# Performance work log

Hardware: AMD Instinct MI355X
Metric: run time of the kernel (lower is better)

The kernel has to match this reference:

```python
import jax, jax.numpy as jnp
import numpy as np
from math import factorial, sqrt

# ---- configuration (matches init_kwargs) ----
MUL = 64
N = 32768
IRREPS1 = [(MUL, l) for l in range(3)]   # 64x0e + 64x1o + 64x2e
IRREPS2 = [(1, l) for l in range(3)]     # 1x0e + 1x1o + 1x2e (spherical harmonics)
IRREPS_OUT = [(MUL, l) for l in range(3)]
# (i_in1, i_in2, i_out) -- all parity/triangle-allowed uvw paths with l<=2
PATHS = [(0,0,0),(0,1,1),(0,2,2),(1,0,1),(1,1,0),(1,1,2),(1,2,1),(2,0,2),(2,1,1),(2,2,0),(2,2,2)]

# ---- real Clebsch-Gordan (e3nn convention: real basis, unit Frobenius norm) ----
def _su2_cg(j1, m1, j2, m2, j3, m3):
    if m3 != m1 + m2:
        return 0.0
    f = factorial
    vmin = max(-j1 + j2 + m3, -j1 + m1, 0)
    vmax = min(j2 + j3 + m1, j3 - j1 + j2, j3 + m3)
    C = sqrt((2*j3+1) * f(j3+j1-j2) * f(j3-j1+j2) * f(j1+j2-j3) * f(j3+m3) * f(j3-m3)
             / (f(j1+j2+j3+1) * f(j1-m1) * f(j1+m1) * f(j2-m2) * f(j2+m2)))
    S = 0.0
    for v in range(vmin, vmax + 1):
        S += (-1.0)**(v + j2 + m2) * f(j2+j3+m1-v) * f(j1-m1+v) / (f(v) * f(j3-j1+j2-v) * f(j3+m3-v) * f(v+j1-j2-m3))
    return C * S

def _su2_clebsch_gordan(j1, j2, j3):
    mat = np.zeros((2*j1+1, 2*j2+1, 2*j3+1))
    for m1 in range(-j1, j1+1):
        for m2 in range(-j2, j2+1):
            if abs(m1 + m2) <= j3:
                mat[j1+m1, j2+m2, j3+m1+m2] = _su2_cg(j1, m1, j2, m2, j3, m1+m2)
    return mat

def _change_basis_real_to_complex(l):
    q = np.zeros((2*l+1, 2*l+1), dtype=np.complex128)
    for m in range(-l, 0):
        q[l+m, l+abs(m)] = 1/sqrt(2)
        q[l+m, l-abs(m)] = -1j/sqrt(2)
    q[l, l] = 1
    for m in range(1, l+1):
        q[l+m, l+abs(m)] = (-1)**m / sqrt(2)
        q[l+m, l-abs(m)] = 1j * (-1)**m / sqrt(2)
    return (-1j)**l * q

def clebsch_gordan(l1, l2, l3):
    Q1 = _change_basis_real_to_complex(l1)
    Q2 = _change_basis_real_to_complex(l2)
    Q3 = _change_basis_real_to_complex(l3)
    C = _su2_clebsch_gordan(l1, l2, l3)
    C = np.einsum('ij,kl,mn,ikn->jlm', Q1, Q2, np.conj(Q3.T), C)
    C = np.real(C)
    return C / np.linalg.norm(C)  # unit Frobenius norm (e3nn convention)

# ---- static layout / path weights ----
def _offsets(irreps):
    offs, s = [], 0
    for mul, l in irreps:
        offs.append(s)
        s += mul * (2*l + 1)
    return offs

OFF1, OFF2, OFFO = _offsets(IRREPS1), _offsets(IRREPS2), _offsets(IRREPS_OUT)
# path_normalization='element', irrep_normalization='component'
_norm = {}
for (i1, i2, io) in PATHS:
    _norm[io] = _norm.get(io, 0) + IRREPS1[i1][0] * IRREPS2[i2][0]
PW = [sqrt((2*IRREPS_OUT[io][1] + 1) / _norm[io]) for (_, _, io) in PATHS]


def setup_inputs() -> dict:
    key = jax.random.key(0)
    k1, k2, k3 = jax.random.split(key, 3)
    dim1 = sum(m * (2*l+1) for m, l in IRREPS1)  # 576
    dim2 = sum(m * (2*l+1) for m, l in IRREPS2)  # 9
    nw = sum(IRREPS1[i1][0] * IRREPS2[i2][0] * IRREPS_OUT[io][0] for (i1, i2, io) in PATHS)
    x1 = jax.random.normal(k1, (N, dim1), dtype=jnp.float32)
    x2 = jax.random.normal(k2, (N, dim2), dtype=jnp.float32)
    weights = jax.random.normal(k3, (nw,), dtype=jnp.float32)
    return {"x1": x1, "x2": x2, "weights": weights}


def reference(x1, x2, weights):
    out_acc = [None] * len(IRREPS_OUT)
    wi = 0
    for (i1, i2, io), pw in zip(PATHS, PW):
        m1, l1 = IRREPS1[i1]
        m2, l2 = IRREPS2[i2]
        mo, lo = IRREPS_OUT[io]
        npar = m1 * m2 * mo
        w = weights[wi:wi + npar].reshape(m1, m2, mo)
        wi += npar
        # per-irrep chunks: [N, mul, 2l+1]
        x1c = x1[:, OFF1[i1]:OFF1[i1] + m1 * (2*l1+1)].reshape(-1, m1, 2*l1+1)
        x2c = x2[:, OFF2[i2]:OFF2[i2] + m2 * (2*l2+1)].reshape(-1, m2, 2*l2+1)
        cg = jnp.asarray(pw * clebsch_gordan(l1, l2, lo), dtype=x1.dtype)
        out = jnp.einsum('uvw,ijk,nui,nvj->nwk', w, cg, x1c, x2c)
        out_acc[io] = out if out_acc[io] is None else out_acc[io] + out
    return jnp.concatenate([o.reshape(o.shape[0], -1) for o in out_acc], axis=1)
```

## Files before the change

kernel.cpp:

```cpp
#include <hip/hip_runtime.h>
#include <hip/hip_bf16.h>

#define NDIM1 576
#define NDIM2 9
#define NDIMO 576

typedef __attribute__((ext_vector_type(8))) short short8;
typedef __attribute__((ext_vector_type(4))) float f32x4;

union U8 { unsigned short s[8]; short8 v; };

__device__ inline unsigned short f2bf(float x) {
  return __builtin_bit_cast(unsigned short, __float2bfloat16(x));
}

constexpr bool cg_nonzero(int m1, int m2, int m3) {
  int a1 = m1 < 0 ? -m1 : m1, a2 = m2 < 0 ? -m2 : m2, a3 = m3 < 0 ? -m3 : m3;
  int d = a1 > a2 ? a1 - a2 : a2 - a1;
  bool mag = (a3 == a1 + a2) || (a3 == d);
  int neg = (m1 < 0) + (m2 < 0) + (m3 < 0);
  return mag && ((neg & 1) == 0);
}

constexpr double cfact(int n) { double r = 1.0; for (int i = 2; i <= n; i++) r *= (double)i; return r; }
constexpr double csqrt_(double x) {
  if (x <= 0.0) return 0.0;
  double g = x < 1.0 ? 1.0 : x;
  for (int i = 0; i < 60; i++) g = 0.5 * (g + x / g);
  return g;
}
constexpr int cmax3(int a, int b, int c) { int m = a > b ? a : b; return m > c ? m : c; }
constexpr int cmin3(int a, int b, int c) { int m = a < b ? a : b; return m < c ? m : c; }

struct cpx { double re; double im; };
constexpr cpx operator*(cpx a, cpx b) { return {a.re * b.re - a.im * b.im, a.re * b.im + a.im * b.re}; }
constexpr cpx operator+(cpx a, cpx b) { return {a.re + b.re, a.im + b.im}; }
constexpr cpx cconj(cpx a) { return {a.re, -a.im}; }
constexpr cpx cscale(cpx a, double s) { return {a.re * s, a.im * s}; }

constexpr double su2_cg_c(int j1, int m1, int j2, int m2, int j3, int m3) {
  if (m3 != m1 + m2) return 0.0;
  int vmin = cmax3(-j1 + j2 + m3, -j1 + m1, 0);
  int vmax = cmin3(j2 + j3 + m1, j3 - j1 + j2, j3 + m3);
  double C = csqrt_((2.0 * j3 + 1.0) * cfact(j3 + j1 - j2) * cfact(j3 - j1 + j2) *
                    cfact(j1 + j2 - j3) * cfact(j3 + m3) * cfact(j3 - m3) /
                    (cfact(j1 + j2 + j3 + 1) * cfact(j1 - m1) * cfact(j1 + m1) *
                     cfact(j2 - m2) * cfact(j2 + m2)));
  double S = 0.0;
  for (int vv = vmin; vv <= vmax; vv++) {
    double sg = ((vv + j2 + m2) & 1) ? -1.0 : 1.0;
    S += sg * cfact(j2 + j3 + m1 - vv) * cfact(j1 - m1 + vv) /
         (cfact(vv) * cfact(j3 - j1 + j2 - vv) * cfact(j3 + m3 - vv) * cfact(vv + j1 - j2 - m3));
  }
  return C * S;
}

struct QM { cpx q[5][5]; };
constexpr QM cb_r2c_c(int l) {
  QM m{};
  const double is2 = 1.0 / csqrt_(2.0);
  for (int mm = -l; mm < 0; mm++) {
    m.q[l + mm][l - mm] = {is2, 0.0};
    m.q[l + mm][l + mm] = {0.0, -is2};
  }
  m.q[l][l] = {1.0, 0.0};
  for (int mm = 1; mm <= l; mm++) {
    double sg = (mm & 1) ? -1.0 : 1.0;
    m.q[l + mm][l + mm] = {sg * is2, 0.0};
    m.q[l + mm][l - mm] = {0.0, sg * is2};
  }
  cpx f{1.0, 0.0};
  for (int t = 0; t < l; t++) f = f * cpx{0.0, -1.0};
  for (int a = 0; a < 2 * l + 1; a++)
    for (int b = 0; b < 2 * l + 1; b++) m.q[a][b] = m.q[a][b] * f;
  return m;
}

struct C555 { double v[5][5][5]; };
constexpr C555 cg_real_c(int l1, int l2, int l3) {
  QM q1 = cb_r2c_c(l1), q2 = cb_r2c_c(l2), q3 = cb_r2c_c(l3);
  double su[5][5][5]{};
  for (int i = 0; i < 2 * l1 + 1; i++)
    for (int k = 0; k < 2 * l2 + 1; k++)
      for (int n = 0; n < 2 * l3 + 1; n++)
        su[i][k][n] = su2_cg_c(l1, i - l1, l2, k - l2, l3, n - l3);
  C555 o{};
  double nrm = 0.0;
  for (int x = 0; x < 2 * l1 + 1; x++)
    for (int y = 0; y < 2 * l2 + 1; y++)
      for (int z = 0; z < 2 * l3 + 1; z++) {
        cpx a{0.0, 0.0};
        for (int i = 0; i < 2 * l1 + 1; i++)
          for (int k = 0; k < 2 * l2 + 1; k++)
            for (int n = 0; n < 2 * l3 + 1; n++) {
              double s = su[i][k][n];
              if (s != 0.0) a = a + cscale(q1.q[i][x] * q2.q[k][y] * cconj(q3.q[n][z]), s);
            }
        o.v[x][y][z] = a.re;
        nrm += a.re * a.re;
      }
  nrm = csqrt_(nrm);
  for (int x = 0; x < 2 * l1 + 1; x++)
    for (int y = 0; y < 2 * l2 + 1; y++)
      for (int z = 0; z < 2 * l3 + 1; z++) o.v[x][y][z] /= nrm;
  return o;
}

static constexpr C555 CGP0 = cg_real_c(0, 0, 0);
static constexpr C555 CGP1 = cg_real_c(0, 1, 1);
static constexpr C555 CGP2 = cg_real_c(0, 2, 2);
static constexpr C555 CGP3 = cg_real_c(1, 0, 1);
static constexpr C555 CGP4 = cg_real_c(1, 1, 0);
static constexpr C555 CGP5 = cg_real_c(1, 1, 2);
static constexpr C555 CGP6 = cg_real_c(1, 2, 1);
static constexpr C555 CGP7 = cg_real_c(2, 0, 2);
static constexpr C555 CGP8 = cg_real_c(2, 1, 1);
static constexpr C555 CGP9 = cg_real_c(2, 2, 0);
static constexpr C555 CGP10 = cg_real_c(2, 2, 2);

struct CGTabC { float v[363]; };
constexpr CGTabC build_flat() {
  CGTabC t{};
  const C555* cp[11] = {&CGP0, &CGP1, &CGP2, &CGP3, &CGP4, &CGP5, &CGP6, &CGP7, &CGP8, &CGP9, &CGP10};
  const int PL1[11] = {0, 0, 0, 1, 1, 1, 1, 2, 2, 2, 2};
  const int PL2[11] = {0, 1, 2, 0, 1, 1, 2, 0, 1, 2, 2};
  const int PLO[11] = {0, 1, 2, 1, 0, 2, 1, 2, 1, 0, 2};
  const int CGO[11] = {0, 1, 10, 35, 44, 53, 98, 143, 168, 213, 238};
  const double pw_io[3] = {csqrt_(1.0 / 192.0), csqrt_(3.0 / 256.0), csqrt_(5.0 / 256.0)};
  for (int p = 0; p < 11; p++) {
    int l1 = PL1[p], l2 = PL2[p], lo = PLO[p];
    double pw = pw_io[lo];
    for (int i = 0; i < 2 * l1 + 1; i++)
      for (int j = 0; j < 2 * l2 + 1; j++)
        for (int k = 0; k < 2 * lo + 1; k++)
          t.v[CGO[p] + (i * (2 * l2 + 1) + j) * (2 * lo + 1) + k] = (float)(pw * cp[p]->v[i][j][k]);
  }
  return t;
}
static constexpr CGTabC CGT = build_flat();

__global__ __launch_bounds__(256) void prep_w_kernel(const float* __restrict__ W,
                                                     short8* __restrict__ wf) {
  int idx = blockIdx.x * 256 + threadIdx.x;
  if (idx >= 11 * 2 * 4 * 64) return;
  int lane = idx & 63;
  int v = (idx >> 6) & 3;
  int s = (idx >> 8) & 1;
  int p = idx >> 9;
  int g = lane >> 4, r16 = lane & 15;
  const float* wp = W + p * 4096 + (s * 32 + g * 8) * 64 + v * 16 + r16;
  U8 u;
#pragma unroll
  for (int t = 0; t < 8; t++) u.s[t] = f2bf(wp[t * 64]);
  wf[idx] = u.v;
}

__device__ __forceinline__ void stage_issue2(const float* __restrict__ x1, int nt,
                                             int wv, int g, int r16, f32x4 (&raw)[20]) {
  const float* row = x1 + (size_t)(nt * 16 + r16) * NDIM1;
  if (wv == 0) {
#pragma unroll
    for (int s = 0; s < 2; s++) {
      const f32x4* p = (const f32x4*)(row + (s * 32 + g * 8));
      raw[s * 2 + 0] = p[0];
      raw[s * 2 + 1] = p[1];
    }
#pragma unroll
    for (int s = 0; s < 2; s++) {
      const f32x4* p = (const f32x4*)(row + 64 + (s * 32 + g * 8) * 3);
#pragma unroll
      for (int q = 0; q < 6; q++) raw[4 + s * 6 + q] = p[q];
    }
  } else {
#pragma unroll
    for (int s = 0; s < 2; s++) {
      const f32x4* p = (const f32x4*)(row + 256 + (s * 32 + g * 8) * 5);
#pragma unroll
      for (int q = 0; q < 10; q++) raw[s * 10 + q] = p[q];
    }
  }
}

__device__ __forceinline__ void stage_write2(short8 (*fb)[64], int wv, int lane,
                                             const f32x4 (&raw)[20]) {
  const float* rf = (const float*)raw;
  if (wv == 0) {
#pragma unroll
    for (int s = 0; s < 2; s++) {
      U8 u;
#pragma unroll
      for (int t = 0; t < 8; t++) u.s[t] = f2bf(rf[s * 8 + t]);
      fb[s][lane] = u.v;
    }
#pragma unroll
    for (int s = 0; s < 2; s++)
#pragma unroll
      for (int i = 0; i < 3; i++) {
        U8 u;
#pragma unroll
        for (int t = 0; t < 8; t++) u.s[t] = f2bf(rf[16 + s * 24 + t * 3 + i]);
        fb[2 + s * 3 + i][lane] = u.v;
      }
  } else {
#pragma unroll
    for (int s = 0; s < 2; s++)
#pragma unroll
      for (int i = 0; i < 5; i++) {
        U8 u;
#pragma unroll
        for (int t = 0; t < 8; t++) u.s[t] = f2bf(rf[s * 40 + t * 5 + i]);
        fb[8 + s * 5 + i][lane] = u.v;
      }
  }
}

template <int NI>
__device__ __forceinline__ void run_path(const short8* __restrict__ wf, int p, int v, int lane,
                                         const short8 (&af)[NI][2], f32x4 (&acc)[NI]) {
#pragma unroll
  for (int i = 0; i < NI; i++) acc[i] = (f32x4){0.f, 0.f, 0.f, 0.f};
#pragma unroll
  for (int s = 0; s < 2; s++) {
    short8 b = wf[((p * 2 + s) * 4 + v) * 64 + lane];
#pragma unroll
    for (int i = 0; i < NI; i++)
      acc[i] = __builtin_amdgcn_mfma_f32_16x16x32_bf16(af[i][s], b, acc[i], 0, 0, 0);
  }
}

template <int L1, int L2, int LO, int CGO, int NI>
__device__ __forceinline__ void epilogue(const f32x4 (&acc)[NI],
                                         const float (&x2v)[4][9], float (&outr)[4][9]) {
  constexpr int JO = (L2 == 0) ? 0 : (L2 == 1 ? 1 : 4);
  constexpr int KO = (LO == 0) ? 0 : (LO == 1 ? 1 : 4);
#pragma unroll
  for (int i = 0; i < 2 * L1 + 1; i++) {
#pragma unroll
    for (int j = 0; j < 2 * L2 + 1; j++) {
#pragma unroll
      for (int k = 0; k < 2 * LO + 1; k++) {
        if (!cg_nonzero(i - L1, j - L2, k - LO)) continue;
        float c = CGT.v[CGO + (i * (2 * L2 + 1) + j) * (2 * LO + 1) + k];
#pragma unroll
        for (int r = 0; r < 4; r++)
          outr[r][KO + k] = fmaf(c * x2v[r][JO + j], acc[i][r], outr[r][KO + k]);
      }
    }
  }
}

__device__ __forceinline__ void compute_tile(const short8 (*fb)[64],
                                             const float* __restrict__ x2,
                                             const short8* __restrict__ wf,
                                             float* __restrict__ out,
                                             int n0, int v, int lane, int g, int r16) {
  f32x4 xv[9];
  {
    const f32x4* p2 = (const f32x4*)(x2 + (size_t)(n0 + g * 4) * NDIM2);
#pragma unroll
    for (int q = 0; q < 9; q++) xv[q] = p2[q];
  }
  float x2v[4][9];
  float outr[4][9];
#pragma unroll
  for (int r = 0; r < 4; r++)
#pragma unroll
    for (int j = 0; j < 9; j++) {
      int idx = r * 9 + j;
      x2v[r][j] = xv[idx >> 2][idx & 3];
      outr[r][j] = 0.f;
    }

  {
    short8 af[1][2]; f32x4 acc[1];
#pragma unroll
    for (int s = 0; s < 2; s++) af[0][s] = fb[s][lane];
    run_path<1>(wf, 0, v, lane, af, acc); epilogue<0, 0, 0, 0, 1>(acc, x2v, outr);
    run_path<1>(wf, 1, v, lane, af, acc); epilogue<0, 1, 1, 1, 1>(acc, x2v, outr);
    run_path<1>(wf, 2, v, lane, af, acc); epilogue<0, 2, 2, 10, 1>(acc, x2v, outr);
  }
  {
    short8 af[3][2]; f32x4 acc[3];
#pragma unroll
    for (int s = 0; s < 2; s++)
#pragma unroll
      for (int i = 0; i < 3; i++) af[i][s] = fb[2 + s * 3 + i][lane];
    run_path<3>(wf, 3, v, lane, af, acc); epilogue<1, 0, 1, 35, 3>(acc, x2v, outr);
    run_path<3>(wf, 4, v, lane, af, acc); epilogue<1, 1, 0, 44, 3>(acc, x2v, outr);
    run_path<3>(wf, 5, v, lane, af, acc); epilogue<1, 1, 2, 53, 3>(acc, x2v, outr);
    run_path<3>(wf, 6, v, lane, af, acc); epilogue<1, 2, 1, 98, 3>(acc, x2v, outr);
  }
  {
    short8 af[5][2]; f32x4 acc[5];
#pragma unroll
    for (int s = 0; s < 2; s++)
#pragma unroll
      for (int i = 0; i < 5; i++) af[i][s] = fb[8 + s * 5 + i][lane];
    run_path<5>(wf, 7, v, lane, af, acc); epilogue<2, 0, 2, 143, 5>(acc, x2v, outr);
    run_path<5>(wf, 8, v, lane, af, acc); epilogue<2, 1, 1, 168, 5>(acc, x2v, outr);
    run_path<5>(wf, 9, v, lane, af, acc); epilogue<2, 2, 0, 213, 5>(acc, x2v, outr);
    run_path<5>(wf, 10, v, lane, af, acc); epilogue<2, 2, 2, 238, 5>(acc, x2v, outr);
  }

  const int w = v * 16 + r16;
#pragma unroll
  for (int r = 0; r < 4; r++) {
    float* op = out + (size_t)(n0 + g * 4 + r) * NDIMO;
    op[w] = outr[r][0];
#pragma unroll
    for (int k = 0; k < 3; k++) op[64 + w * 3 + k] = outr[r][1 + k];
#pragma unroll
    for (int k = 0; k < 5; k++) op[256 + w * 5 + k] = outr[r][4 + k];
  }
}

__global__ __launch_bounds__(128) void TPWithWeights_44925357916441_kernel(
    const float* __restrict__ x1, const float* __restrict__ x2,
    const short8* __restrict__ wf, float* __restrict__ out) {
  __shared__ short8 frg[18][64];

  const int lane = threadIdx.x & 63;
  const int wv = threadIdx.x >> 6;
  const int g = lane >> 4, r16 = lane & 15;
  const int n0 = blockIdx.x << 4;

  {
    f32x4 raw[20];
    stage_issue2(x1, blockIdx.x, wv, g, r16, raw);
    stage_write2(frg, wv, lane, raw);
  }
  __syncthreads();

  compute_tile(frg, x2, wf, out, n0, wv * 2 + 0, lane, g, r16);
  compute_tile(frg, x2, wf, out, n0, wv * 2 + 1, lane, g, r16);
}

extern "C" void kernel_launch(void* const* d_in, const int* in_sizes, int n_in,
                              void* d_out, int out_size, void* d_ws, size_t ws_size,
                              hipStream_t stream) {
  const float* x1 = (const float*)d_in[0];
  const float* x2 = (const float*)d_in[1];
  const float* W  = (const float*)d_in[2];
  float* out = (float*)d_out;

  int N = in_sizes[0] / NDIM1;

  short8* wf = (short8*)d_ws;

  hipLaunchKernelGGL(prep_w_kernel, dim3(22), dim3(256), 0, stream, W, wf);
  hipLaunchKernelGGL(TPWithWeights_44925357916441_kernel, dim3(N / 16), dim3(128), 0,
                     stream, x1, x2, wf, out);
}
```

Baseline: 52.63 us.

## Split output-channel quarters across single-wave blocks and drop LDS staging

Each 64-thread block now handles one 16-row tile and one quarter of the output channels. Each wave loads and converts the x1 fragments it needs straight from global memory into registers, replacing the two-wave shared-memory staging and the barrier. This removes LDS traffic and synchronisation and gives the scheduler four times as many independent waves. In exchange, every x1 row is now read from global memory four times (once per channel quarter), relying on the cache to absorb the repeats. The tile index is hardcoded with the mask 2047 and shift 11, which assumes exactly 2048 tiles.

```diff
diff --git a/kernel.cpp b/kernel.cpp
--- a/kernel.cpp
+++ b/kernel.cpp
@@ -155,62 +155,31 @@
   wf[idx] = u.v;
 }
 
-__device__ __forceinline__ void stage_issue2(const float* __restrict__ x1, int nt,
-                                             int wv, int g, int r16, f32x4 (&raw)[20]) {
-  const float* row = x1 + (size_t)(nt * 16 + r16) * NDIM1;
-  if (wv == 0) {
-#pragma unroll
-    for (int s = 0; s < 2; s++) {
-      const f32x4* p = (const f32x4*)(row + (s * 32 + g * 8));
-      raw[s * 2 + 0] = p[0];
-      raw[s * 2 + 1] = p[1];
+template <int NI>
+__device__ __forceinline__ void issue_x1(const float* __restrict__ row, int g,
+                                         f32x4 (&raw)[4 * NI]) {
+#pragma unroll
+  for (int s = 0; s < 2; s++) {
+    const f32x4* src = (const f32x4*)(row + (s * 32 + g * 8) * NI);
+#pragma unroll
+    for (int q = 0; q < 2 * NI; q++) raw[s * 2 * NI + q] = src[q];
+  }
+}
+
+template <int NI>
+__device__ __forceinline__ void convert_x1(const f32x4 (&raw)[4 * NI], short8 (&af)[NI][2]) {
+#pragma unroll
+  for (int s = 0; s < 2; s++) {
+#pragma unroll
+    for (int i = 0; i < NI; i++) {
+      U8 u;
+#pragma unroll
+      for (int t = 0; t < 8; t++) {
+        int idx = t * NI + i;
+        u.s[t] = f2bf(raw[s * 2 * NI + (idx >> 2)][idx & 3]);
+      }
+      af[i][s] = u.v;
     }
-#pragma unroll
-    for (int s = 0; s < 2; s++) {
-      const f32x4* p = (const f32x4*)(row + 64 + (s * 32 + g * 8) * 3);
-#pragma unroll
-      for (int q = 0; q < 6; q++) raw[4 + s * 6 + q] = p[q];
-    }
-  } else {
-#pragma unroll
-    for (int s = 0; s < 2; s++) {
-      const f32x4* p = (const f32x4*)(row + 256 + (s * 32 + g * 8) * 5);
-#pragma unroll
-      for (int q = 0; q < 10; q++) raw[s * 10 + q] = p[q];
-    }
-  }
-}
-
-__device__ __forceinline__ void stage_write2(short8 (*fb)[64], int wv, int lane,
-                                             const f32x4 (&raw)[20]) {
-  const float* rf = (const float*)raw;
-  if (wv == 0) {
-#pragma unroll
-    for (int s = 0; s < 2; s++) {
-      U8 u;
-#pragma unroll
-      for (int t = 0; t < 8; t++) u.s[t] = f2bf(rf[s * 8 + t]);
-      fb[s][lane] = u.v;
-    }
-#pragma unroll
-    for (int s = 0; s < 2; s++)
-#pragma unroll
-      for (int i = 0; i < 3; i++) {
-        U8 u;
-#pragma unroll
-        for (int t = 0; t < 8; t++) u.s[t] = f2bf(rf[16 + s * 24 + t * 3 + i]);
-        fb[2 + s * 3 + i][lane] = u.v;
-      }
-  } else {
-#pragma unroll
-    for (int s = 0; s < 2; s++)
-#pragma unroll
-      for (int i = 0; i < 5; i++) {
-        U8 u;
-#pragma unroll
-        for (int t = 0; t < 8; t++) u.s[t] = f2bf(rf[s * 40 + t * 5 + i]);
-        fb[8 + s * 5 + i][lane] = u.v;
-      }
   }
 }
 
@@ -249,17 +218,31 @@
   }
 }
 
-__device__ __forceinline__ void compute_tile(const short8 (*fb)[64],
-                                             const float* __restrict__ x2,
-                                             const short8* __restrict__ wf,
-                                             float* __restrict__ out,
-                                             int n0, int v, int lane, int g, int r16) {
-  f32x4 xv[9];
+__global__ __launch_bounds__(64) void TPWithWeights_44925357916441_kernel(
+    const float* __restrict__ x1, const float* __restrict__ x2,
+    const short8* __restrict__ wf, float* __restrict__ out) {
+  const int lane = threadIdx.x;
+  const int g = lane >> 4, r16 = lane & 15;
+  const int tile = blockIdx.x & 2047;
+  const int v = blockIdx.x >> 11;
+  const int n0 = tile << 4;
+  const float* rowbase = x1 + (size_t)(n0 + r16) * NDIM1;
+
+  f32x4 raw0[4], raw1[12], raw2[20], xv[9];
+  issue_x1<1>(rowbase + 0, g, raw0);
+  issue_x1<3>(rowbase + 64, g, raw1);
+  issue_x1<5>(rowbase + 256, g, raw2);
   {
     const f32x4* p2 = (const f32x4*)(x2 + (size_t)(n0 + g * 4) * NDIM2);
 #pragma unroll
     for (int q = 0; q < 9; q++) xv[q] = p2[q];
   }
+
+  short8 af0[1][2], af1[3][2], af2[5][2];
+  convert_x1<1>(raw0, af0);
+  convert_x1<3>(raw1, af1);
+  convert_x1<5>(raw2, af2);
+
   float x2v[4][9];
   float outr[4][9];
 #pragma unroll
@@ -272,34 +255,24 @@
     }
 
   {
-    short8 af[1][2]; f32x4 acc[1];
-#pragma unroll
-    for (int s = 0; s < 2; s++) af[0][s] = fb[s][lane];
-    run_path<1>(wf, 0, v, lane, af, acc); epilogue<0, 0, 0, 0, 1>(acc, x2v, outr);
-    run_path<1>(wf, 1, v, lane, af, acc); epilogue<0, 1, 1, 1, 1>(acc, x2v, outr);
-    run_path<1>(wf, 2, v, lane, af, acc); epilogue<0, 2, 2, 10, 1>(acc, x2v, outr);
+    f32x4 acc[1];
+    run_path<1>(wf, 0, v, lane, af0, acc); epilogue<0, 0, 0, 0, 1>(acc, x2v, outr);
+    run_path<1>(wf, 1, v, lane, af0, acc); epilogue<0, 1, 1, 1, 1>(acc, x2v, outr);
+    run_path<1>(wf, 2, v, lane, af0, acc); epilogue<0, 2, 2, 10, 1>(acc, x2v, outr);
   }
   {
-    short8 af[3][2]; f32x4 acc[3];
-#pragma unroll
-    for (int s = 0; s < 2; s++)
-#pragma unroll
-      for (int i = 0; i < 3; i++) af[i][s] = fb[2 + s * 3 + i][lane];
-    run_path<3>(wf, 3, v, lane, af, acc); epilogue<1, 0, 1, 35, 3>(acc, x2v, outr);
-    run_path<3>(wf, 4, v, lane, af, acc); epilogue<1, 1, 0, 44, 3>(acc, x2v, outr);
-    run_path<3>(wf, 5, v, lane, af, acc); epilogue<1, 1, 2, 53, 3>(acc, x2v, outr);
-    run_path<3>(wf, 6, v, lane, af, acc); epilogue<1, 2, 1, 98, 3>(acc, x2v, outr);
+    f32x4 acc[3];
+    run_path<3>(wf, 3, v, lane, af1, acc); epilogue<1, 0, 1, 35, 3>(acc, x2v, outr);
+    run_path<3>(wf, 4, v, lane, af1, acc); epilogue<1, 1, 0, 44, 3>(acc, x2v, outr);
+    run_path<3>(wf, 5, v, lane, af1, acc); epilogue<1, 1, 2, 53, 3>(acc, x2v, outr);
+    run_path<3>(wf, 6, v, lane, af1, acc); epilogue<1, 2, 1, 98, 3>(acc, x2v, outr);
   }
   {
-    short8 af[5][2]; f32x4 acc[5];
-#pragma unroll
-    for (int s = 0; s < 2; s++)
-#pragma unroll
-      for (int i = 0; i < 5; i++) af[i][s] = fb[8 + s * 5 + i][lane];
-    run_path<5>(wf, 7, v, lane, af, acc); epilogue<2, 0, 2, 143, 5>(acc, x2v, outr);
-    run_path<5>(wf, 8, v, lane, af, acc); epilogue<2, 1, 1, 168, 5>(acc, x2v, outr);
-    run_path<5>(wf, 9, v, lane, af, acc); epilogue<2, 2, 0, 213, 5>(acc, x2v, outr);
-    run_path<5>(wf, 10, v, lane, af, acc); epilogue<2, 2, 2, 238, 5>(acc, x2v, outr);
+    f32x4 acc[5];
+    run_path<5>(wf, 7, v, lane, af2, acc); epilogue<2, 0, 2, 143, 5>(acc, x2v, outr);
+    run_path<5>(wf, 8, v, lane, af2, acc); epilogue<2, 1, 1, 168, 5>(acc, x2v, outr);
+    run_path<5>(wf, 9, v, lane, af2, acc); epilogue<2, 2, 0, 213, 5>(acc, x2v, outr);
+    run_path<5>(wf, 10, v, lane, af2, acc); epilogue<2, 2, 2, 238, 5>(acc, x2v, outr);
   }
 
   const int w = v * 16 + r16;
@@ -312,27 +285,6 @@
 #pragma unroll
     for (int k = 0; k < 5; k++) op[256 + w * 5 + k] = outr[r][4 + k];
   }
-}
-
-__global__ __launch_bounds__(128) void TPWithWeights_44925357916441_kernel(
-    const float* __restrict__ x1, const float* __restrict__ x2,
-    const short8* __restrict__ wf, float* __restrict__ out) {
-  __shared__ short8 frg[18][64];
-
-  const int lane = threadIdx.x & 63;
-  const int wv = threadIdx.x >> 6;
-  const int g = lane >> 4, r16 = lane & 15;
-  const int n0 = blockIdx.x << 4;
-
-  {
-    f32x4 raw[20];
-    stage_issue2(x1, blockIdx.x, wv, g, r16, raw);
-    stage_write2(frg, wv, lane, raw);
-  }
-  __syncthreads();
-
-  compute_tile(frg, x2, wf, out, n0, wv * 2 + 0, lane, g, r16);
-  compute_tile(frg, x2, wf, out, n0, wv * 2 + 1, lane, g, r16);
 }
 
 extern "C" void kernel_launch(void* const* d_in, const int* in_sizes, int n_in,
@@ -344,10 +296,11 @@
   float* out = (float*)d_out;
 
   int N = in_sizes[0] / NDIM1;
+  int ntiles = N / 16;
 
   short8* wf = (short8*)d_ws;
 
   hipLaunchKernelGGL(prep_w_kernel, dim3(22), dim3(256), 0, stream, W, wf);
-  hipLaunchKernelGGL(TPWithWeights_44925357916441_kernel, dim3(N / 16), dim3(128), 0,
+  hipLaunchKernelGGL(TPWithWeights_44925357916441_kernel, dim3(ntiles * 4), dim3(64), 0,
                      stream, x1, x2, wf, out);
 }
```

Result: slower. 72.48 us (+37.7%).
